# Optimization experiments

Measured on AMD Instinct MI355X. Metric: run time of the kernel, lower is better.

The kernel has to match this reference:

```python
import jax, jax.numpy as jnp
import numpy as np
from jax import lax

B, T, V, E, H, K = 64, 512, 30000, 256, 256, 9


def setup_inputs() -> dict:
    key = jax.random.key(0)
    ks = jax.random.split(key, 15)
    s = 0.08
    return {
        "word_inputs": jax.random.randint(ks[0], (B, T), 0, V),
        "word_seq_lengths": jax.random.randint(ks[1], (B,), 1, T + 1),
        "seq_token_label": jax.random.randint(ks[2], (B, T), 0, K),
        "word_vec": jax.random.normal(ks[3], (V, E), jnp.float32) * s,
        "W_ih_f": jax.random.normal(ks[4], (4 * H, E), jnp.float32) * s,
        "W_hh_f": jax.random.normal(ks[5], (4 * H, H), jnp.float32) * s,
        "b_f": jax.random.normal(ks[6], (4 * H,), jnp.float32) * s,
        "W_ih_b": jax.random.normal(ks[7], (4 * H, E), jnp.float32) * s,
        "W_hh_b": jax.random.normal(ks[8], (4 * H, H), jnp.float32) * s,
        "b_b": jax.random.normal(ks[9], (4 * H,), jnp.float32) * s,
        "W_out": jax.random.normal(ks[10], (K, 2 * H), jnp.float32) * s,
        "b_out": jax.random.normal(ks[11], (K,), jnp.float32) * s,
        "start_trans": jax.random.normal(ks[12], (K,), jnp.float32) * s,
        "end_trans": jax.random.normal(ks[13], (K,), jnp.float32) * s,
        "trans": jax.random.normal(ks[14], (K, K), jnp.float32) * s,
    }


def _lstm_dir(x, W_ih, W_hh, b):
    # x: [B,T,E] -> h: [B,T,H]; torch gate order (i, f, g, o)
    gx = jnp.einsum('bte,ge->btg', x, W_ih) + b  # input projection hoisted out of scan
    h0 = jnp.zeros((x.shape[0], W_hh.shape[1]), x.dtype)

    def step(carry, g_t):
        h, c = carry
        g = g_t + h @ W_hh.T
        i, f, gg, o = jnp.split(g, 4, axis=-1)
        c = jax.nn.sigmoid(f) * c + jax.nn.sigmoid(i) * jnp.tanh(gg)
        h = jax.nn.sigmoid(o) * jnp.tanh(c)
        return (h, c), h

    _, hs = lax.scan(step, (h0, h0), jnp.swapaxes(gx, 0, 1))
    return jnp.swapaxes(hs, 0, 1)


def reference(word_inputs, word_seq_lengths, seq_token_label, word_vec,
              W_ih_f, W_hh_f, b_f, W_ih_b, W_hh_b, b_b,
              W_out, b_out, start_trans, end_trans, trans):
    t_idx = jnp.arange(T)
    mask = t_idx[None, :] < word_seq_lengths[:, None]  # [B,T] bool (pack_padded semantics)
    # index map that reverses the valid prefix of each sequence (involution)
    rev_idx = jnp.where(mask, word_seq_lengths[:, None] - 1 - t_idx[None, :], t_idx[None, :])

    emb = word_vec[word_inputs]  # [B,T,E]
    h_fwd = _lstm_dir(emb, W_ih_f, W_hh_f, b_f)
    emb_rev = jnp.take_along_axis(emb, rev_idx[:, :, None], axis=1)
    h_bwd = jnp.take_along_axis(_lstm_dir(emb_rev, W_ih_b, W_hh_b, b_b), rev_idx[:, :, None], axis=1)
    feats = jnp.concatenate([h_fwd, h_bwd], axis=-1) * mask[:, :, None]  # [B,T,2H]
    emissions = feats @ W_out.T + b_out  # [B,T,K]

    mf = mask.astype(emissions.dtype)
    # ---- CRF numerator (score of gold path) ----
    emit_sc = jnp.take_along_axis(emissions, seq_token_label[:, :, None], 2)[:, :, 0]  # [B,T]
    num = start_trans[seq_token_label[:, 0]] + emit_sc[:, 0]
    trans_sc = trans[seq_token_label[:, :-1], seq_token_label[:, 1:]]  # [B,T-1]
    num = num + jnp.sum((trans_sc + emit_sc[:, 1:]) * mf[:, 1:], axis=1)
    last_tags = jnp.take_along_axis(seq_token_label, (word_seq_lengths - 1)[:, None], 1)[:, 0]
    num = num + end_trans[last_tags]

    # ---- CRF log-partition (alpha recursion) ----
    em_t = jnp.swapaxes(emissions[:, 1:], 0, 1)  # [T-1,B,K]
    mk_t = jnp.swapaxes(mask[:, 1:], 0, 1)       # [T-1,B]
    score0 = start_trans[None, :] + emissions[:, 0]  # [B,K]

    def alpha_step(score, inp):
        e_t, m_t = inp
        nxt = jax.nn.logsumexp(score[:, :, None] + trans[None], axis=1) + e_t
        return jnp.where(m_t[:, None], nxt, score), None

    scoreZ, _ = lax.scan(alpha_step, score0, (em_t, mk_t))
    denom = jax.nn.logsumexp(scoreZ + end_trans[None, :], axis=1)
    ner_loss = -jnp.mean(num - denom)  # reduction='mean' over batch, negated

    # ---- Viterbi decode ----
    def vit_step(score, inp):
        e_t, m_t = inp
        tot = score[:, :, None] + trans[None]  # [B,K,K]
        best_prev = jnp.argmax(tot, axis=1)    # [B,K]
        nxt = jnp.max(tot, axis=1) + e_t
        return jnp.where(m_t[:, None], nxt, score), best_prev

    scoreV, hist = lax.scan(vit_step, score0, (em_t, mk_t))  # hist [T-1,B,K]
    best_last = jnp.argmax(scoreV + end_trans[None, :], axis=1)  # [B]

    def back_step(cur, inp):
        h_t, m_t = inp
        new = jnp.take_along_axis(h_t, cur[:, None], 1)[:, 0]
        cur = jnp.where(m_t, new, cur)
        return cur, cur

    _, preds_rev = lax.scan(back_step, best_last, (hist[::-1], mk_t[::-1]))  # [T-1,B]
    preds = jnp.concatenate([jnp.swapaxes(preds_rev[::-1], 0, 1), best_last[:, None]], axis=1)  # [B,T]
    preds = jnp.where(mask, preds, 0)

    return ner_loss, preds, feats
```

## Files before the change

### kernel.cpp

```cpp
#include <hip/hip_runtime.h>
#include <hip/hip_bf16.h>
#include <math.h>

#ifndef __has_builtin
#define __has_builtin(x) 0
#endif

typedef unsigned int uint;
typedef unsigned short ushort;
typedef _Float16 half2_t __attribute__((ext_vector_type(2)));

#define PREG 96
#define WREG_UINTS (PREG * 2 * 512)
#define WLDS_UINTS (16 * 512 * 4)

__device__ __forceinline__ float sigm(float x) {
    return __fdividef(1.0f, 1.0f + __expf(-x));
}
__device__ __forceinline__ float tanh_fast(float x) {
    float sg = __fdividef(1.0f, 1.0f + __expf(-2.0f * x));
    return sg + sg - 1.0f;
}
__device__ __forceinline__ float dot2f(uint w, uint h, float acc) {
#if __has_builtin(__builtin_amdgcn_fdot2)
    return __builtin_amdgcn_fdot2(__builtin_bit_cast(half2_t, w),
                                  __builtin_bit_cast(half2_t, h), acc, false);
#else
    half2_t a = __builtin_bit_cast(half2_t, w);
    half2_t b = __builtin_bit_cast(half2_t, h);
    return acc + (float)a.x * (float)b.x + (float)a.y * (float)b.y;
#endif
}
__device__ __forceinline__ uint packh2(float a, float b) {
    ushort u0 = __builtin_bit_cast(ushort, (_Float16)a);
    ushort u1 = __builtin_bit_cast(ushort, (_Float16)b);
    return (uint)u0 | ((uint)u1 << 16);
}

#define R96(X) \
  X(0) X(1) X(2) X(3) X(4) X(5) X(6) X(7) \
  X(8) X(9) X(10) X(11) X(12) X(13) X(14) X(15) \
  X(16) X(17) X(18) X(19) X(20) X(21) X(22) X(23) \
  X(24) X(25) X(26) X(27) X(28) X(29) X(30) X(31) \
  X(32) X(33) X(34) X(35) X(36) X(37) X(38) X(39) \
  X(40) X(41) X(42) X(43) X(44) X(45) X(46) X(47) \
  X(48) X(49) X(50) X(51) X(52) X(53) X(54) X(55) \
  X(56) X(57) X(58) X(59) X(60) X(61) X(62) X(63) \
  X(64) X(65) X(66) X(67) X(68) X(69) X(70) X(71) \
  X(72) X(73) X(74) X(75) X(76) X(77) X(78) X(79) \
  X(80) X(81) X(82) X(83) X(84) X(85) X(86) X(87) \
  X(88) X(89) X(90) X(91) X(92) X(93) X(94) X(95)

#define R16(X) \
  X(0) X(1) X(2) X(3) X(4) X(5) X(6) X(7) \
  X(8) X(9) X(10) X(11) X(12) X(13) X(14) X(15)

#define WDECL(m) uint wA##m, wB##m;
#define WLOAD(m) wA##m = wreg[(2 * (m)) * 512 + tid]; \
                 wB##m = wreg[(2 * (m) + 1) * 512 + tid];
#define WSTEP(m) { \
    uint hp = (uint)__builtin_amdgcn_readlane((int)((m) < 64 ? r0 : r1), (m) & 63); \
    aA = dot2f(wA##m, hp, aA); \
    aB = dot2f(wB##m, hp, aB); }
#define LSTEP(i) { \
    uint4 w4 = reinterpret_cast<const uint4*>(lw)[((i) << 9) + tid]; \
    uint hp0 = (uint)__builtin_amdgcn_readlane((int)r1, 32 + 2 * (i)); \
    uint hp1 = (uint)__builtin_amdgcn_readlane((int)r1, 33 + 2 * (i)); \
    aA = dot2f(w4.x, hp0, aA); \
    aB = dot2f(w4.y, hp0, aB); \
    aA = dot2f(w4.z, hp1, aA); \
    aB = dot2f(w4.w, hp1, aB); }

__global__ __launch_bounds__(256) void zero_kernel(float* __restrict__ out,
                                                   const int* __restrict__ lens) {
    int bid = blockIdx.x;
    if (bid < 65536) {
        int g = bid * 256 + threadIdx.x;
        int row = g >> 9;
        int t = row & 511;
        int b = row >> 9;
        if (t >= lens[b]) out[32769 + g] = 0.0f;
    } else if (bid < 65536 + 128) {
        int p = (bid - 65536) * 256 + threadIdx.x;
        out[1 + p] = 0.0f;
    } else if (threadIdx.x == 0) {
        out[0] = 0.0f;
    }
}

__global__ __launch_bounds__(256) void pack_kernel(const float* __restrict__ WF,
                                                   const float* __restrict__ WB,
                                                   uint* __restrict__ wregF,
                                                   uint* __restrict__ wregB,
                                                   uint* __restrict__ wldsF,
                                                   uint* __restrict__ wldsB) {
    int id = blockIdx.x * 256 + threadIdx.x;
    const float* W = WF; uint* wr = wregF; uint* wl = wldsF;
    if (id >= 131072) { id -= 131072; W = WB; wr = wregB; wl = wldsB; }
    int m, x, tl, dst_lds = 0, id2 = 0;
    if (id < WREG_UINTS) {
        m = id >> 10;
        int r = id & 1023;
        x = r >> 9;
        tl = r & 511;
    } else {
        id2 = id - WREG_UINTS;
        int c = id2 & 3;
        int u = id2 >> 2;
        tl = u & 511;
        int g = u >> 9;
        m = PREG + 2 * g + (c >> 1);
        x = c & 1;
        dst_lds = 1;
    }
    int j = tl >> 1, s = tl & 1;
    int q = (s << 1) + x;
    const float* row = W + ((size_t)((q << 8) + j) << 8);
    uint pk = packh2(row[2 * m], row[2 * m + 1]);
    if (dst_lds) wl[id2] = pk;
    else         wr[((m << 1) + x) * 512 + tl] = pk;
}

__global__ __launch_bounds__(256) void wih_pack_kernel(const float* __restrict__ WihF,
                                                       const float* __restrict__ WihB,
                                                       uint* __restrict__ w16F,
                                                       uint* __restrict__ w16B) {
    int id = blockIdx.x * 256 + threadIdx.x;
    const float* W = WihF; uint* dst = w16F;
    if (id >= 131072) { id -= 131072; W = WihB; dst = w16B; }
    int col = id >> 7;
    int p = id & 127;
    int perm = ((col & 3) << 8) + (col >> 2);
    const float* row = W + ((size_t)perm << 8);
    dst[(col << 7) + p] = packh2(row[2 * p], row[2 * p + 1]);
}

__global__ __launch_bounds__(256) void gemm_gx_kernel(const int* __restrict__ widx,
                                                      const int* __restrict__ lens,
                                                      const float* __restrict__ wvec,
                                                      const uint* __restrict__ wih16,
                                                      const float* __restrict__ bias,
                                                      _Float16* __restrict__ gx) {
    int row0 = blockIdx.x * 64;
    int b = row0 >> 9;
    int t0 = row0 & 511;
    if (t0 >= lens[b]) return;
    int n0 = blockIdx.y * 64;

    __shared__ __align__(16) uint As[16][68];
    __shared__ __align__(16) uint Bs[16][68];
    __shared__ int aoff[64];

    int tid = threadIdx.x;
    if (tid < 64) aoff[tid] = widx[row0 + tid] << 8;
    __syncthreads();

    float acc[4][4] = {};
    int tn = tid & 15, tm = tid >> 4;

    for (int k0p = 0; k0p < 128; k0p += 16) {
#pragma unroll
        for (int p = 0; p < 4; ++p) {
            int lin = p * 256 + tid;
            int kp = lin & 15, m = lin >> 4;
            const float2 av = *reinterpret_cast<const float2*>(
                &wvec[aoff[m] + ((k0p + kp) << 1)]);
            As[kp][m] = packh2(av.x, av.y);
            Bs[kp][m] = wih16[((n0 + m) << 7) + k0p + kp];
        }
        __syncthreads();
#pragma unroll
        for (int kp = 0; kp < 16; ++kp) {
            uint4 a4 = *reinterpret_cast<const uint4*>(&As[kp][tm * 4]);
            uint4 b4 = *reinterpret_cast<const uint4*>(&Bs[kp][tn * 4]);
            uint am[4] = {a4.x, a4.y, a4.z, a4.w};
            uint bn[4] = {b4.x, b4.y, b4.z, b4.w};
#pragma unroll
            for (int i = 0; i < 4; ++i)
#pragma unroll
                for (int j = 0; j < 4; ++j) acc[i][j] = dot2f(am[i], bn[j], acc[i][j]);
        }
        __syncthreads();
    }

#pragma unroll
    for (int i = 0; i < 4; ++i) {
        int row = row0 + tm * 4 + i;
        ushort u[4];
#pragma unroll
        for (int j = 0; j < 4; ++j) {
            int col = n0 + tn * 4 + j;
            int perm = ((col & 3) << 8) + (col >> 2);
            u[j] = __builtin_bit_cast(ushort, (_Float16)(acc[i][j] + bias[perm]));
        }
        uint2 st;
        st.x = (uint)u[0] | ((uint)u[1] << 16);
        st.y = (uint)u[2] | ((uint)u[3] << 16);
        *reinterpret_cast<uint2*>(&gx[row * 1024 + n0 + tn * 4]) = st;
    }
}

__global__ __launch_bounds__(512, 2)
void lstm_kernel(const _Float16* __restrict__ gx0,
                 const _Float16* __restrict__ gx1,
                 const uint* __restrict__ wreg0,
                 const uint* __restrict__ wreg1,
                 const uint* __restrict__ wlds0,
                 const uint* __restrict__ wlds1,
                 const int* __restrict__ lens,
                 float* __restrict__ feats) {
    int dir = blockIdx.x & 1;
    int b = blockIdx.x >> 1;
    const uint* gxu = reinterpret_cast<const uint*>(dir ? gx1 : gx0) + ((size_t)(b << 9) << 9);
    const uint* wreg = dir ? wreg1 : wreg0;
    const uint* wlds = dir ? wlds1 : wlds0;
    int len = lens[b];
    int tid = threadIdx.x;
    int lane = tid & 63;
    int sg = tid & 1;

    __shared__ __align__(16) uint lw[WLDS_UINTS];
    __shared__ __align__(16) uint hpair[2][128];

    for (int i = tid; i < WLDS_UINTS; i += 512) lw[i] = wlds[i];

    R96(WDECL)
    R96(WLOAD)
    __syncthreads();

    float c = 0.0f;
    uint r0 = 0, r1 = 0;
    int pp = 0;

    int t0i = dir ? (len - 1) : 0;
    uint g = gxu[(t0i << 9) + tid];

    for (int tp = 0; tp < len; ++tp) {
        int t = dir ? (len - 1 - tp) : tp;
        int tnn = dir ? (len - 2 - tp) : (tp + 1);
        tnn = tnn < 0 ? 0 : (tnn >= len ? len - 1 : tnn);
        uint gnext = gxu[(tnn << 9) + tid];

        half2_t gv = __builtin_bit_cast(half2_t, g);
        float aA = (float)gv.x;
        float aB = (float)gv.y;

        R96(WSTEP)
        R16(LSTEP)

        float y = sg ? aA + aA : aA;
        float sgm = __fdividef(1.0f, 1.0f + __expf(-y));
        float pA = sg ? sgm + sgm - 1.0f : sgm;
        float pB = sigm(aB);

        float oA = __shfl_xor(pA, 1);
        float oB = __shfl_xor(pB, 1);
        float si = sg ? oA : pA;
        float sf = sg ? oB : pB;
        float tg = sg ? pA : oA;
        float so = sg ? pB : oB;

        c = sf * c + si * tg;
        float h = so * tanh_fast(c);

        if (!sg) {
            reinterpret_cast<ushort*>(hpair[pp])[tid >> 1] =
                __builtin_bit_cast(ushort, (_Float16)h);
        }
        __syncthreads();
        if (!sg) {
            feats[(size_t)(((b << 9) + t)) * 512 + (dir << 8) + (tid >> 1)] = h;
        }
        r0 = hpair[pp][lane];
        r1 = hpair[pp][64 + lane];
        pp ^= 1;
        g = gnext;
    }
}

__global__ __launch_bounds__(64) void emis_kernel(const float* __restrict__ feats,
                                                  const float* __restrict__ Wout,
                                                  const float* __restrict__ bout,
                                                  const int* __restrict__ lens,
                                                  float* __restrict__ emis) {
    int r = blockIdx.x;
    int b = r >> 9, t = r & 511;
    if (t >= lens[b]) return;
    int lane = threadIdx.x;
    const float* fr = feats + (size_t)r * 512;
    float f[8];
#pragma unroll
    for (int i = 0; i < 8; ++i) f[i] = fr[i * 64 + lane];
#pragma unroll
    for (int k = 0; k < 9; ++k) {
        float p = 0.0f;
#pragma unroll
        for (int i = 0; i < 8; ++i) p = fmaf(f[i], Wout[k * 512 + i * 64 + lane], p);
#pragma unroll
        for (int off = 32; off; off >>= 1) p += __shfl_down(p, off);
        if (lane == 0) emis[r * 9 + k] = p + bout[k];
    }
}

__global__ __launch_bounds__(64) void crf_kernel(const float* __restrict__ emis,
                                                 const int* __restrict__ lens,
                                                 const int* __restrict__ labels,
                                                 const float* __restrict__ start_trans,
                                                 const float* __restrict__ end_trans,
                                                 const float* __restrict__ trans,
                                                 float* __restrict__ out) {
    int b = blockIdx.x;
    int len = lens[b];
    int lane = threadIdx.x;
    __shared__ float alpha[9], vit[9];
    __shared__ unsigned char hist[512 * 9];
    const float* eb = emis + b * 512 * 9;
    const int* lb = labels + b * 512;

    float tr[9];
    if (lane < 9) {
#pragma unroll
        for (int i = 0; i < 9; ++i) tr[i] = trans[i * 9 + lane];
        float s0 = start_trans[lane] + eb[lane];
        alpha[lane] = s0;
        vit[lane] = s0;
    }
    __syncthreads();

    for (int t = 1; t < len; ++t) {
        float na = 0.0f, nv = 0.0f;
        if (lane < 9) {
            float e = eb[t * 9 + lane];
            float a[9];
#pragma unroll
            for (int i = 0; i < 9; ++i) a[i] = alpha[i] + tr[i];
            float m = a[0];
#pragma unroll
            for (int i = 1; i < 9; ++i) m = fmaxf(m, a[i]);
            float s = 0.0f;
#pragma unroll
            for (int i = 0; i < 9; ++i) s += __expf(a[i] - m);
            na = m + __logf(s) + e;
            float bv = vit[0] + tr[0];
            int bi = 0;
#pragma unroll
            for (int i = 1; i < 9; ++i) {
                float x = vit[i] + tr[i];
                if (x > bv) { bv = x; bi = i; }
            }
            nv = bv + e;
            hist[t * 9 + lane] = (unsigned char)bi;
        }
        __syncthreads();
        if (lane < 9) { alpha[lane] = na; vit[lane] = nv; }
        __syncthreads();
    }

    float part = 0.0f;
    for (int t = 1 + lane; t < len; t += 64) {
        int yp = lb[t - 1], y = lb[t];
        part += trans[yp * 9 + y] + eb[t * 9 + y];
    }
#pragma unroll
    for (int off = 32; off; off >>= 1) part += __shfl_down(part, off);

    if (lane == 0) {
        int y0 = lb[0];
        float num = start_trans[y0] + eb[y0] + part + end_trans[lb[len - 1]];
        float m = alpha[0] + end_trans[0];
        for (int j = 1; j < 9; ++j) m = fmaxf(m, alpha[j] + end_trans[j]);
        float s = 0.0f;
        for (int j = 0; j < 9; ++j) s += __expf(alpha[j] + end_trans[j] - m);
        float denom = m + __logf(s);
        atomicAdd(out, (denom - num) * (1.0f / 64.0f));

        float bm = vit[0] + end_trans[0];
        int cur = 0;
        for (int j = 1; j < 9; ++j) {
            float x = vit[j] + end_trans[j];
            if (x > bm) { bm = x; cur = j; }
        }
        float* preds = out + 1 + b * 512;
        preds[len - 1] = (float)cur;
        for (int t = len - 1; t >= 1; --t) {
            cur = hist[t * 9 + cur];
            preds[t - 1] = (float)cur;
        }
    }
}

extern "C" void kernel_launch(void* const* d_in, const int* in_sizes, int n_in,
                              void* d_out, int out_size, void* d_ws, size_t ws_size,
                              hipStream_t stream) {
    const int* widx = (const int*)d_in[0];
    const int* lens = (const int*)d_in[1];
    const int* labels = (const int*)d_in[2];
    const float* wvec = (const float*)d_in[3];
    const float* WihF = (const float*)d_in[4];
    const float* WhhF = (const float*)d_in[5];
    const float* bF = (const float*)d_in[6];
    const float* WihB = (const float*)d_in[7];
    const float* WhhB = (const float*)d_in[8];
    const float* bB = (const float*)d_in[9];
    const float* Wout = (const float*)d_in[10];
    const float* bout = (const float*)d_in[11];
    const float* start_trans = (const float*)d_in[12];
    const float* end_trans = (const float*)d_in[13];
    const float* trans9 = (const float*)d_in[14];
    float* out = (float*)d_out;
    char* ws = (char*)d_ws;

    _Float16* gxF = (_Float16*)(ws);
    _Float16* gxB = (_Float16*)(ws + 67108864);
    uint* wregF   = (uint*)(ws + 134217728);
    uint* wregB   = (uint*)(ws + 134610944);
    uint* wldsF   = (uint*)(ws + 135004160);
    uint* wldsB   = (uint*)(ws + 135135232);
    uint* wih16F  = (uint*)(ws + 135266304);
    uint* wih16B  = (uint*)(ws + 135790592);
    float* emis   = (float*)(ws + 135266304);
    (void)in_sizes; (void)n_in; (void)out_size; (void)ws_size;

    float* feats = out + 1 + 32768;

    zero_kernel<<<65665, 256, 0, stream>>>(out, lens);
    pack_kernel<<<1024, 256, 0, stream>>>(WhhF, WhhB, wregF, wregB, wldsF, wldsB);
    wih_pack_kernel<<<1024, 256, 0, stream>>>(WihF, WihB, wih16F, wih16B);

    dim3 ggrid(512, 16);
    gemm_gx_kernel<<<ggrid, 256, 0, stream>>>(widx, lens, wvec, wih16F, bF, gxF);
    gemm_gx_kernel<<<ggrid, 256, 0, stream>>>(widx, lens, wvec, wih16B, bB, gxB);

    lstm_kernel<<<128, 512, 0, stream>>>(gxF, gxB, wregF, wregB, wldsF, wldsB, lens, feats);

    emis_kernel<<<32768, 64, 0, stream>>>(feats, Wout, bout, lens, emis);
    crf_kernel<<<64, 64, 0, stream>>>(emis, lens, labels, start_trans, end_trans, trans9, out);
}
```

Before: 1.665 ms.

## Split recurrent weights across registers, LDS and streamed global loads

The recurrent weight matrix was split 96 pairs in registers and 32 pairs in LDS. It is now split 34 pairs in registers, 38 in LDS and 56 streamed from global/L2 each timestep. The streamed part uses software-pipelined double-buffered uint4 loads interleaved with the register and LDS dot products. The aim is to cut register pressure (dropping the launch bound's occupancy hint) while hiding streamed-load latency behind compute. The risk is that every timestep now re-reads a large weight slice from cache, which adds global memory traffic and latency to the serial recurrence.

```diff
diff --git a/kernel.cpp b/kernel.cpp
--- a/kernel.cpp
+++ b/kernel.cpp
@@ -10,9 +10,9 @@
 typedef unsigned short ushort;
 typedef _Float16 half2_t __attribute__((ext_vector_type(2)));
 
-#define PREG 96
-#define WREG_UINTS (PREG * 2 * 512)
-#define WLDS_UINTS (16 * 512 * 4)
+#define WREG_UINTS (34 * 2 * 512)
+#define WLDS_U4    (19 * 512)
+#define WSTR_U4    (28 * 512)
 
 __device__ __forceinline__ float sigm(float x) {
     return __fdividef(1.0f, 1.0f + __expf(-x));
@@ -37,39 +37,44 @@
     return (uint)u0 | ((uint)u1 << 16);
 }
 
-#define R96(X) \
+#define R34(X) \
   X(0) X(1) X(2) X(3) X(4) X(5) X(6) X(7) \
   X(8) X(9) X(10) X(11) X(12) X(13) X(14) X(15) \
   X(16) X(17) X(18) X(19) X(20) X(21) X(22) X(23) \
   X(24) X(25) X(26) X(27) X(28) X(29) X(30) X(31) \
-  X(32) X(33) X(34) X(35) X(36) X(37) X(38) X(39) \
-  X(40) X(41) X(42) X(43) X(44) X(45) X(46) X(47) \
-  X(48) X(49) X(50) X(51) X(52) X(53) X(54) X(55) \
-  X(56) X(57) X(58) X(59) X(60) X(61) X(62) X(63) \
-  X(64) X(65) X(66) X(67) X(68) X(69) X(70) X(71) \
-  X(72) X(73) X(74) X(75) X(76) X(77) X(78) X(79) \
-  X(80) X(81) X(82) X(83) X(84) X(85) X(86) X(87) \
-  X(88) X(89) X(90) X(91) X(92) X(93) X(94) X(95)
-
-#define R16(X) \
-  X(0) X(1) X(2) X(3) X(4) X(5) X(6) X(7) \
-  X(8) X(9) X(10) X(11) X(12) X(13) X(14) X(15)
+  X(32) X(33)
 
 #define WDECL(m) uint wA##m, wB##m;
 #define WLOAD(m) wA##m = wreg[(2 * (m)) * 512 + tid]; \
                  wB##m = wreg[(2 * (m) + 1) * 512 + tid];
 #define WSTEP(m) { \
-    uint hp = (uint)__builtin_amdgcn_readlane((int)((m) < 64 ? r0 : r1), (m) & 63); \
+    uint hp = (uint)__builtin_amdgcn_readlane((int)r0, (m)); \
     aA = dot2f(wA##m, hp, aA); \
     aB = dot2f(wB##m, hp, aB); }
 #define LSTEP(i) { \
-    uint4 w4 = reinterpret_cast<const uint4*>(lw)[((i) << 9) + tid]; \
-    uint hp0 = (uint)__builtin_amdgcn_readlane((int)r1, 32 + 2 * (i)); \
-    uint hp1 = (uint)__builtin_amdgcn_readlane((int)r1, 33 + 2 * (i)); \
+    uint4 w4 = lw4[(i) * 512 + tid]; \
+    uint hp0 = (uint)__builtin_amdgcn_readlane( \
+        (int)((34 + 2 * (i)) < 64 ? r0 : r1), (34 + 2 * (i)) & 63); \
+    uint hp1 = (uint)__builtin_amdgcn_readlane( \
+        (int)((35 + 2 * (i)) < 64 ? r0 : r1), (35 + 2 * (i)) & 63); \
     aA = dot2f(w4.x, hp0, aA); \
     aB = dot2f(w4.y, hp0, aB); \
     aA = dot2f(w4.z, hp1, aA); \
     aB = dot2f(w4.w, hp1, aB); }
+#define SISSUE(a, b, c, d, k0) { \
+    a = wstr4[((k0) + 0) * 512 + tid]; \
+    b = wstr4[((k0) + 1) * 512 + tid]; \
+    c = wstr4[((k0) + 2) * 512 + tid]; \
+    d = wstr4[((k0) + 3) * 512 + tid]; }
+#define SPAIR(u, k) { \
+    uint hp0 = (uint)__builtin_amdgcn_readlane((int)r1, 8 + 2 * (k)); \
+    uint hp1 = (uint)__builtin_amdgcn_readlane((int)r1, 9 + 2 * (k)); \
+    aA = dot2f(u.x, hp0, aA); \
+    aB = dot2f(u.y, hp0, aB); \
+    aA = dot2f(u.z, hp1, aA); \
+    aB = dot2f(u.w, hp1, aB); }
+#define SCONS(a, b, c, d, k0) \
+    SPAIR(a, (k0) + 0) SPAIR(b, (k0) + 1) SPAIR(c, (k0) + 2) SPAIR(d, (k0) + 3)
 
 __global__ __launch_bounds__(256) void zero_kernel(float* __restrict__ out,
                                                    const int* __restrict__ lens) {
@@ -93,32 +98,29 @@
                                                    uint* __restrict__ wregF,
                                                    uint* __restrict__ wregB,
                                                    uint* __restrict__ wldsF,
-                                                   uint* __restrict__ wldsB) {
+                                                   uint* __restrict__ wldsB,
+                                                   uint* __restrict__ wstrF,
+                                                   uint* __restrict__ wstrB) {
     int id = blockIdx.x * 256 + threadIdx.x;
-    const float* W = WF; uint* wr = wregF; uint* wl = wldsF;
-    if (id >= 131072) { id -= 131072; W = WB; wr = wregB; wl = wldsB; }
-    int m, x, tl, dst_lds = 0, id2 = 0;
-    if (id < WREG_UINTS) {
-        m = id >> 10;
-        int r = id & 1023;
-        x = r >> 9;
-        tl = r & 511;
-    } else {
-        id2 = id - WREG_UINTS;
-        int c = id2 & 3;
-        int u = id2 >> 2;
-        tl = u & 511;
-        int g = u >> 9;
-        m = PREG + 2 * g + (c >> 1);
-        x = c & 1;
-        dst_lds = 1;
-    }
+    const float* W = WF; uint* wr = wregF; uint* wl = wldsF; uint* wsp = wstrF;
+    if (id >= 131072) { id -= 131072; W = WB; wr = wregB; wl = wldsB; wsp = wstrB; }
+    int m = id >> 10;
+    int r = id & 1023;
+    int x = r >> 9;
+    int tl = r & 511;
     int j = tl >> 1, s = tl & 1;
     int q = (s << 1) + x;
     const float* row = W + ((size_t)((q << 8) + j) << 8);
     uint pk = packh2(row[2 * m], row[2 * m + 1]);
-    if (dst_lds) wl[id2] = pk;
-    else         wr[((m << 1) + x) * 512 + tl] = pk;
+    if (m < 34) {
+        wr[((m << 1) + x) * 512 + tl] = pk;
+    } else if (m < 72) {
+        int mL = m - 34;
+        wl[(((mL >> 1) << 9) + tl) * 4 + ((mL & 1) << 1) + x] = pk;
+    } else {
+        int mS = m - 72;
+        wsp[(((mS >> 1) << 9) + tl) * 4 + ((mS & 1) << 1) + x] = pk;
+    }
 }
 
 __global__ __launch_bounds__(256) void wih_pack_kernel(const float* __restrict__ WihF,
@@ -200,32 +202,35 @@
     }
 }
 
-__global__ __launch_bounds__(512, 2)
+__global__ __launch_bounds__(512)
 void lstm_kernel(const _Float16* __restrict__ gx0,
                  const _Float16* __restrict__ gx1,
                  const uint* __restrict__ wreg0,
                  const uint* __restrict__ wreg1,
                  const uint* __restrict__ wlds0,
                  const uint* __restrict__ wlds1,
+                 const uint* __restrict__ wstr0,
+                 const uint* __restrict__ wstr1,
                  const int* __restrict__ lens,
                  float* __restrict__ feats) {
     int dir = blockIdx.x & 1;
     int b = blockIdx.x >> 1;
     const uint* gxu = reinterpret_cast<const uint*>(dir ? gx1 : gx0) + ((size_t)(b << 9) << 9);
     const uint* wreg = dir ? wreg1 : wreg0;
-    const uint* wlds = dir ? wlds1 : wlds0;
+    const uint4* wlds4 = reinterpret_cast<const uint4*>(dir ? wlds1 : wlds0);
+    const uint4* wstr4 = reinterpret_cast<const uint4*>(dir ? wstr1 : wstr0);
     int len = lens[b];
     int tid = threadIdx.x;
     int lane = tid & 63;
     int sg = tid & 1;
 
-    __shared__ __align__(16) uint lw[WLDS_UINTS];
+    __shared__ __align__(16) uint4 lw4[WLDS_U4];
     __shared__ __align__(16) uint hpair[2][128];
 
-    for (int i = tid; i < WLDS_UINTS; i += 512) lw[i] = wlds[i];
-
-    R96(WDECL)
-    R96(WLOAD)
+    for (int i = tid; i < WLDS_U4; i += 512) lw4[i] = wlds4[i];
+
+    R34(WDECL)
+    R34(WLOAD)
     __syncthreads();
 
     float c = 0.0f;
@@ -245,8 +250,32 @@
         float aA = (float)gv.x;
         float aB = (float)gv.y;
 
-        R96(WSTEP)
-        R16(LSTEP)
+        uint4 sA0, sA1, sA2, sA3;
+        uint4 sB0, sB1, sB2, sB3;
+
+        SISSUE(sA0, sA1, sA2, sA3, 0)
+        WSTEP(0)  WSTEP(1)  WSTEP(2)  WSTEP(3)  WSTEP(4)  WSTEP(5)
+        WSTEP(6)  WSTEP(7)  WSTEP(8)  WSTEP(9)  WSTEP(10) WSTEP(11)
+        WSTEP(12) WSTEP(13) WSTEP(14) WSTEP(15) WSTEP(16)
+        SISSUE(sB0, sB1, sB2, sB3, 4)
+        SCONS(sA0, sA1, sA2, sA3, 0)
+        WSTEP(17) WSTEP(18) WSTEP(19) WSTEP(20) WSTEP(21) WSTEP(22)
+        WSTEP(23) WSTEP(24) WSTEP(25) WSTEP(26) WSTEP(27) WSTEP(28)
+        WSTEP(29) WSTEP(30) WSTEP(31) WSTEP(32) WSTEP(33)
+        SISSUE(sA0, sA1, sA2, sA3, 8)
+        SCONS(sB0, sB1, sB2, sB3, 4)
+        LSTEP(0) LSTEP(1) LSTEP(2) LSTEP(3) LSTEP(4) LSTEP(5) LSTEP(6)
+        SISSUE(sB0, sB1, sB2, sB3, 12)
+        SCONS(sA0, sA1, sA2, sA3, 8)
+        LSTEP(7) LSTEP(8) LSTEP(9) LSTEP(10) LSTEP(11) LSTEP(12)
+        SISSUE(sA0, sA1, sA2, sA3, 16)
+        SCONS(sB0, sB1, sB2, sB3, 12)
+        LSTEP(13) LSTEP(14) LSTEP(15) LSTEP(16) LSTEP(17) LSTEP(18)
+        SISSUE(sB0, sB1, sB2, sB3, 20)
+        SCONS(sA0, sA1, sA2, sA3, 16)
+        SISSUE(sA0, sA1, sA2, sA3, 24)
+        SCONS(sB0, sB1, sB2, sB3, 20)
+        SCONS(sA0, sA1, sA2, sA3, 24)
 
         float y = sg ? aA + aA : aA;
         float sgm = __fdividef(1.0f, 1.0f + __expf(-y));
@@ -413,9 +442,11 @@
     _Float16* gxF = (_Float16*)(ws);
     _Float16* gxB = (_Float16*)(ws + 67108864);
     uint* wregF   = (uint*)(ws + 134217728);
-    uint* wregB   = (uint*)(ws + 134610944);
-    uint* wldsF   = (uint*)(ws + 135004160);
-    uint* wldsB   = (uint*)(ws + 135135232);
+    uint* wregB   = (uint*)(ws + 134356992);
+    uint* wldsF   = (uint*)(ws + 134496256);
+    uint* wldsB   = (uint*)(ws + 134651904);
+    uint* wstrF   = (uint*)(ws + 134807552);
+    uint* wstrB   = (uint*)(ws + 135036928);
     uint* wih16F  = (uint*)(ws + 135266304);
     uint* wih16B  = (uint*)(ws + 135790592);
     float* emis   = (float*)(ws + 135266304);
@@ -424,14 +455,16 @@
     float* feats = out + 1 + 32768;
 
     zero_kernel<<<65665, 256, 0, stream>>>(out, lens);
-    pack_kernel<<<1024, 256, 0, stream>>>(WhhF, WhhB, wregF, wregB, wldsF, wldsB);
+    pack_kernel<<<1024, 256, 0, stream>>>(WhhF, WhhB, wregF, wregB, wldsF, wldsB,
+                                          wstrF, wstrB);
     wih_pack_kernel<<<1024, 256, 0, stream>>>(WihF, WihB, wih16F, wih16B);
 
     dim3 ggrid(512, 16);
     gemm_gx_kernel<<<ggrid, 256, 0, stream>>>(widx, lens, wvec, wih16F, bF, gxF);
     gemm_gx_kernel<<<ggrid, 256, 0, stream>>>(widx, lens, wvec, wih16B, bB, gxB);
 
-    lstm_kernel<<<128, 512, 0, stream>>>(gxF, gxB, wregF, wregB, wldsF, wldsB, lens, feats);
+    lstm_kernel<<<128, 512, 0, stream>>>(gxF, gxB, wregF, wregB, wldsF, wldsB,
+                                         wstrF, wstrB, lens, feats);
 
     emis_kernel<<<32768, 64, 0, stream>>>(feats, Wout, bout, lens, emis);
     crf_kernel<<<64, 64, 0, stream>>>(emis, lens, labels, start_trans, end_trans, trans9, out);
```

Measured after the change: 1.640 ms. No clear change (-1.5%).
